# Kernel optimization log

Measured on AMD Instinct MI355X. Metric: run time of the kernel, lower is better.

The kernel has to match this reference:

```python
import jax, jax.numpy as jnp
import numpy as np

N_NODES = 50000
N_EDGES = 800000
D_IN = 128
D_HID = 128
N_CLS = 40


def setup_inputs() -> dict:
    key = jax.random.key(0)
    ks = jax.random.split(key, 9)
    x = jax.random.normal(ks[0], (N_NODES, D_IN), dtype=jnp.float32)
    edge_index = jax.random.randint(ks[1], (2, N_EDGES), 0, N_NODES, dtype=jnp.int64)
    def lin(k, fan_in, fan_out):
        bound = 1.0 / np.sqrt(fan_in)
        return jax.random.uniform(k, (fan_in, fan_out), jnp.float32, -bound, bound)
    params = {
        'w1_l': lin(ks[2], D_IN, D_HID), 'w1_r': lin(ks[3], D_IN, D_HID),
        'b1': jnp.zeros((D_HID,), jnp.float32),
        'w2_l': lin(ks[4], D_HID, D_HID), 'w2_r': lin(ks[5], D_HID, D_HID),
        'b2': jnp.zeros((D_HID,), jnp.float32),
        'w3_l': lin(ks[6], D_HID, N_CLS), 'w3_r': lin(ks[7], D_HID, N_CLS),
        'b3': jnp.zeros((N_CLS,), jnp.float32),
    }
    return {'x': x, 'edge_index': edge_index, **params}


def _sage_layer(x, src, dst, w_l, w_r, b):
    # mean-aggregate messages from src -> dst, then lin_l(agg) + lin_r(x) + b, relu
    msgs = x[src]                                             # [E, d] gather
    agg = jax.ops.segment_sum(msgs, dst, num_segments=x.shape[0])  # [N, d]
    deg = jax.ops.segment_sum(jnp.ones((src.shape[0],), x.dtype), dst,
                              num_segments=x.shape[0])        # [N]
    agg = agg / jnp.maximum(deg, 1.0)[:, None]
    out = agg @ w_l + x @ w_r + b
    return jax.nn.relu(out)  # dropout p=0.0 -> identity


def reference(x, edge_index, w1_l, w1_r, b1, w2_l, w2_r, b2, w3_l, w3_r, b3):
    src, dst = edge_index[0], edge_index[1]
    h = _sage_layer(x, src, dst, w1_l, w1_r, b1)
    h = _sage_layer(h, src, dst, w2_l, w2_r, b2)
    h = _sage_layer(h, src, dst, w3_l, w3_r, b3)
    return h
```

## Files before the change

kernel.cpp:

```cpp
#include <hip/hip_runtime.h>
#include <hip/hip_bf16.h>

#define NN 50000
#define NE 800000
#define DD 128
#define NCLS 40
#define NBK ((NN + 255) >> 8)
#define EPB 1024
#define PB ((NE + EPB - 1) / EPB)
#define CVB ((NN * DD / 4) / 256)
#define WB 384
#define SEMAX 5120

typedef _Float16 f16x8 __attribute__((ext_vector_type(8)));
typedef _Float16 f16x4 __attribute__((ext_vector_type(4)));
typedef float f32x4 __attribute__((ext_vector_type(4)));

__device__ __forceinline__ unsigned int pack2h(_Float16 a, _Float16 b) {
    union { _Float16 h[2]; unsigned int u; } c;
    c.h[0] = a; c.h[1] = b;
    return c.u;
}
__device__ __forceinline__ void unpack2h(unsigned int p, float& a, float& b) {
    union { unsigned int u; _Float16 h[2]; } c;
    c.u = p;
    a = (float)c.h[0]; b = (float)c.h[1];
}

__global__ void k_front(const int* __restrict__ ei, int* __restrict__ cellcnt,
                        int* __restrict__ celloff, unsigned int* __restrict__ pairs,
                        const float* __restrict__ x, unsigned short* __restrict__ xh,
                        const float* __restrict__ w1l, const float* __restrict__ w1r,
                        const float* __restrict__ w2l, const float* __restrict__ w2r,
                        const float* __restrict__ w3l, const float* __restrict__ w3r,
                        unsigned short* __restrict__ bt1h,
                        unsigned short* __restrict__ bt2h,
                        unsigned short* __restrict__ bt3h) {
    if (blockIdx.x >= PB + CVB) {
        int idx = blockIdx.x - (PB + CVB);
        int w = idx >> 1, half = idx & 1;
        int ks = w & 7, tmp = w >> 3;
        int nt = tmp & 7, layer = tmp >> 3;
        const int NT = (layer == 2) ? 3 : 8;
        const int NC = (layer == 2) ? NCLS : DD;
        if (nt >= NT) return;
        const float* wl = (layer == 0) ? w1l : (layer == 1) ? w2l : w3l;
        const float* wr = (layer == 0) ? w1r : (layer == 1) ? w2r : w3r;
        unsigned short* bh = (layer == 0) ? bt1h : (layer == 1) ? bt2h : bt3h;
        int t = threadIdx.x;
        int j = t & 7, lane = (t >> 3) + half * 32;
        int row = nt * 16 + (lane & 15);
        int k = ks * 32 + (lane >> 4) * 8 + j;
        float v = 0.f;
        if (row < NC)
            v = (k < 128) ? wl[(size_t)k * NC + row] : wr[(size_t)(k - 128) * NC + row];
        union { _Float16 f; unsigned short u; } ch;
        ch.f = (_Float16)v;
        bh[((size_t)(ks * NT + nt) * 64 + lane) * 8 + j] = ch.u;
        return;
    }
    if (blockIdx.x >= PB) {
        int i = (blockIdx.x - PB) * 256 + threadIdx.x;
        float4 v = ((const float4*)x)[i];
        f16x4 h;
        h[0] = (_Float16)v.x; h[1] = (_Float16)v.y;
        h[2] = (_Float16)v.z; h[3] = (_Float16)v.w;
        *(f16x4*)(xh + (size_t)i * 4) = h;
        return;
    }
    __shared__ int hist[NBK];
    __shared__ int s[256];
    __shared__ unsigned int sE[EPB];
    __shared__ int nz;
    const int t = threadIdx.x, blk = blockIdx.x;
    const int e0 = blk * EPB;
    if (t == 0) nz = 0;
    for (int i = t; i < NBK; i += 256) hist[i] = 0;
    __syncthreads();
    int any = 0;
    for (int i = t; i < EPB; i += 256)
        if (ei[2 * e0 + 2 * i + 1] != 0) any = 1;
    if (any) atomicOr(&nz, 1);
    __syncthreads();
    const int is64 = (nz == 0);
    unsigned int v[EPB / 256];
    int eb[EPB / 256], er[EPB / 256];
#pragma unroll
    for (int j = 0; j < EPB / 256; ++j) {
        int e = e0 + j * 256 + t;
        if (e < NE) {
            int sv, d;
            if (is64) { sv = ei[2 * e]; d = ei[2 * (NE + e)]; }
            else      { sv = ei[e];     d = ei[NE + e]; }
            v[j] = ((unsigned)sv << 16) | (unsigned)d;
            eb[j] = d >> 8;
            er[j] = atomicAdd(&hist[eb[j]], 1);
        } else {
            eb[j] = -1;
        }
    }
    __syncthreads();
    int hv = (t < NBK) ? hist[t] : 0;
    s[t] = hv;
    __syncthreads();
#pragma unroll
    for (int off = 1; off < 256; off <<= 1) {
        int u = (t >= off) ? s[t - off] : 0;
        __syncthreads();
        s[t] += u;
        __syncthreads();
    }
#pragma unroll
    for (int j = 0; j < EPB / 256; ++j)
        if (eb[j] >= 0) sE[s[eb[j]] - hist[eb[j]] + er[j]] = v[j];
    __syncthreads();
    ((uint4*)(pairs + (size_t)blk * EPB))[t] = ((const uint4*)sE)[t];
    for (int i = t; i < NBK; i += 256) {
        cellcnt[(size_t)i * PB + blk] = hist[i];
        celloff[(size_t)i * PB + blk] = s[i] - hist[i];
    }
}

__global__ void k_scan_ba(const int* __restrict__ cellcnt, int* __restrict__ bsum) {
    __shared__ int red[256];
    int b = blockIdx.x, t = threadIdx.x;
    int acc = 0;
    for (int i = t; i < PB; i += 256) acc += cellcnt[(size_t)b * PB + i];
    red[t] = acc;
    __syncthreads();
#pragma unroll
    for (int off = 128; off > 0; off >>= 1) {
        if (t < off) red[t] += red[t + off];
        __syncthreads();
    }
    if (t == 0) bsum[b] = red[0];
}

__global__ void k_fill2(const unsigned int* __restrict__ pairs,
                        const int* __restrict__ cellcnt,
                        const int* __restrict__ celloff,
                        const int* __restrict__ bsum,
                        int* __restrict__ row_ptr, int* __restrict__ srcs) {
    __shared__ unsigned int sE[SEMAX];
    __shared__ int hist[256];
    __shared__ int cur[256];
    __shared__ int sb[256];
    __shared__ int scnt;
    const int b = blockIdx.x, t = threadIdx.x;
    if (t < 256) {
        int v = (t < NBK) ? bsum[t] : 0;
        sb[t] = v;
    }
    if (t == 0) scnt = 0;
    if (t < 256) hist[t] = 0;
    __syncthreads();
#pragma unroll
    for (int off = 1; off < 256; off <<= 1) {
        int u = (t >= off && t < 256) ? sb[t - off] : 0;
        __syncthreads();
        if (t < 256) sb[t] += u;
        __syncthreads();
    }
    const int bbase = (b == 0) ? 0 : sb[b - 1];
    if (b == NBK - 1 && t == 0) row_ptr[NN] = sb[NBK - 1];
    for (int blk = t; blk < PB; blk += 512) {
        int cnt = cellcnt[(size_t)b * PB + blk];
        if (cnt) {
            int off = celloff[(size_t)b * PB + blk];
            int base = atomicAdd(&scnt, cnt);
            if (base + cnt <= SEMAX) {
                const unsigned int* pp = pairs + (size_t)blk * EPB + off;
                for (int j = 0; j < cnt; ++j) {
                    unsigned int v = pp[j];
                    sE[base + j] = v;
                    atomicAdd(&hist[v & 255u], 1);
                }
            }
        }
    }
    __syncthreads();
    int h = (t < 256) ? hist[t] : 0;
    if (t < 256) cur[t] = h;
    __syncthreads();
#pragma unroll
    for (int off = 1; off < 256; off <<= 1) {
        int u = (t >= off && t < 256) ? cur[t - off] : 0;
        __syncthreads();
        if (t < 256) cur[t] += u;
        __syncthreads();
    }
    if (t < 256) {
        int node = (b << 8) + t;
        int base = bbase + cur[t] - h;
        if (node < NN) row_ptr[node] = base;
        cur[t] = base;
    }
    __syncthreads();
    int total = min(scnt, SEMAX);
    for (int i = t; i < total; i += 512) {
        unsigned int v = sE[i];
        int pos = atomicAdd(&cur[v & 255u], 1);
        srcs[pos] = (int)(v >> 16);
    }
}

__global__ void k_agg(const unsigned int* __restrict__ inh, const int* __restrict__ row_ptr,
                      const int* __restrict__ srcs, unsigned int* __restrict__ oh) {
    int node = blockIdx.x * 4 + (threadIdx.x >> 6);
    if (node >= NN) return;
    int lane = threadIdx.x & 63;
    int b = row_ptr[node], e = row_ptr[node + 1];
    float a0 = 0.f, a1 = 0.f;
    int nfull = (e - b) & ~7;
    int i = b;
    for (; i < b + nfull; i += 8) {
        unsigned int p0 = inh[(size_t)srcs[i + 0] * 64 + lane];
        unsigned int p1 = inh[(size_t)srcs[i + 1] * 64 + lane];
        unsigned int p2 = inh[(size_t)srcs[i + 2] * 64 + lane];
        unsigned int p3 = inh[(size_t)srcs[i + 3] * 64 + lane];
        unsigned int p4 = inh[(size_t)srcs[i + 4] * 64 + lane];
        unsigned int p5 = inh[(size_t)srcs[i + 5] * 64 + lane];
        unsigned int p6 = inh[(size_t)srcs[i + 6] * 64 + lane];
        unsigned int p7 = inh[(size_t)srcs[i + 7] * 64 + lane];
        float u0, u1;
        unpack2h(p0, u0, u1); a0 += u0; a1 += u1;
        unpack2h(p1, u0, u1); a0 += u0; a1 += u1;
        unpack2h(p2, u0, u1); a0 += u0; a1 += u1;
        unpack2h(p3, u0, u1); a0 += u0; a1 += u1;
        unpack2h(p4, u0, u1); a0 += u0; a1 += u1;
        unpack2h(p5, u0, u1); a0 += u0; a1 += u1;
        unpack2h(p6, u0, u1); a0 += u0; a1 += u1;
        unpack2h(p7, u0, u1); a0 += u0; a1 += u1;
    }
    int rem = e - i;
    if (rem > 0) {
        unsigned int p[8];
#pragma unroll
        for (int j = 0; j < 8; ++j) {
            int idx = i + j;
            if (idx > e - 1) idx = e - 1;
            p[j] = inh[(size_t)srcs[idx] * 64 + lane];
        }
#pragma unroll
        for (int j = 0; j < 8; ++j) {
            float u0, u1;
            unpack2h(p[j], u0, u1);
            if (j < rem) { a0 += u0; a1 += u1; }
        }
    }
    int deg = e - b;
    float inv = 1.0f / (float)(deg > 0 ? deg : 1);
    oh[(size_t)node * 64 + lane] = pack2h((_Float16)(a0 * inv), (_Float16)(a1 * inv));
}

template <int NT, int KPS, bool PACKOUT>
__launch_bounds__(256, 4)
__global__ void k_mfma(const unsigned short* __restrict__ A1h,
                       const unsigned short* __restrict__ A2h,
                       const unsigned short* __restrict__ Bthf,
                       const float* __restrict__ bias, float* __restrict__ outf,
                       unsigned short* __restrict__ outh, const int NC) {
    constexpr int STAGE_ELEMS = KPS * NT * 64 * 8;
    constexpr int STAGE_U4 = STAGE_ELEMS / 8;
    __shared__ unsigned short sBh[STAGE_ELEMS];

    const int tid = threadIdx.x;
    const int wave = tid >> 6, lane = tid & 63;
    const int quad = lane >> 4, mr = lane & 15;
    const int m0 = blockIdx.x * 64 + wave * 16;
    const int row = m0 + mr;
    const bool rok = row < NN;

    f32x4 acc[NT] = {};
    const f16x8 zero = {};

    auto aload = [&](int ks) -> f16x8 {
        const int ko = ((ks * 32) & 127) + quad * 8;
        const unsigned short* base = (ks < 4) ? A1h : A2h;
        return rok ? *(const f16x8*)(base + (size_t)row * 128 + ko) : zero;
    };

    f16x8 cah = aload(0), pah;

#pragma unroll
    for (int s = 0; s < 8 / KPS; ++s) {
        const uint4* gh = (const uint4*)(Bthf + (size_t)s * STAGE_ELEMS);
        uint4* lh = (uint4*)sBh;
        if (s) __syncthreads();
        for (int i = tid; i < STAGE_U4; i += 256) lh[i] = gh[i];
        __syncthreads();

#pragma unroll
        for (int kl = 0; kl < KPS; ++kl) {
            const int ks = s * KPS + kl;
            if (ks < 7) pah = aload(ks + 1);
#pragma unroll
            for (int n = 0; n < NT; ++n) {
                const int fo = ((kl * NT + n) * 64 + lane) * 8;
                f16x8 bh = *(const f16x8*)(sBh + fo);
                acc[n] = __builtin_amdgcn_mfma_f32_16x16x32_f16(cah, bh, acc[n], 0, 0, 0);
            }
            cah = pah;
        }
    }

#pragma unroll
    for (int n = 0; n < NT; ++n) {
        int col = n * 16 + mr;
        float bv = (col < NC) ? bias[col] : 0.f;
#pragma unroll
        for (int r = 0; r < 4; ++r) {
            int orow = m0 + quad * 4 + r;
            if (orow < NN && col < NC) {
                float v = acc[n][r] + bv;
                v = v > 0.f ? v : 0.f;
                if (PACKOUT) {
                    union { _Float16 f; unsigned short u; } ch;
                    ch.f = (_Float16)v;
                    outh[(size_t)orow * 128 + col] = ch.u;
                } else {
                    outf[(size_t)orow * NC + col] = v;
                }
            }
        }
    }
}

extern "C" void kernel_launch(void* const* d_in, const int* in_sizes, int n_in,
                              void* d_out, int out_size, void* d_ws, size_t ws_size,
                              hipStream_t stream) {
    const float* x    = (const float*)d_in[0];
    const int*   ei   = (const int*)d_in[1];
    const float* w1_l = (const float*)d_in[2];
    const float* w1_r = (const float*)d_in[3];
    const float* b1   = (const float*)d_in[4];
    const float* w2_l = (const float*)d_in[5];
    const float* w2_r = (const float*)d_in[6];
    const float* b2   = (const float*)d_in[7];
    const float* w3_l = (const float*)d_in[8];
    const float* w3_r = (const float*)d_in[9];
    const float* b3   = (const float*)d_in[10];
    float* out = (float*)d_out;

    char* w = (char*)d_ws;
    size_t off = 0;
    auto alloc = [&](size_t bytes) -> void* {
        void* p = w + off;
        off += (bytes + 255) / 256 * 256;
        return p;
    };
    int* row_ptr = (int*)alloc((size_t)(NN + 1) * 4);
    int* srcs    = (int*)alloc((size_t)NE * 4);
    int* cellcnt = (int*)alloc((size_t)NBK * PB * 4);
    int* celloff = (int*)alloc((size_t)NBK * PB * 4);
    int* bsum    = (int*)alloc((size_t)NBK * 4);
    unsigned int* pairs = (unsigned int*)alloc((size_t)PB * EPB * 4);
    unsigned short* xh   = (unsigned short*)alloc((size_t)NN * DD * 2);
    unsigned short* aggh = (unsigned short*)alloc((size_t)NN * DD * 2);
    unsigned short* h1h  = (unsigned short*)alloc((size_t)NN * DD * 2);
    unsigned short* bt1h = (unsigned short*)alloc((size_t)8 * 8 * 64 * 8 * 2);
    unsigned short* bt2h = (unsigned short*)alloc((size_t)8 * 8 * 64 * 8 * 2);
    unsigned short* bt3h = (unsigned short*)alloc((size_t)8 * 3 * 64 * 8 * 2);
    unsigned short* h2h = xh;
    (void)ws_size;

    k_front<<<PB + CVB + WB, 256, 0, stream>>>(ei, cellcnt, celloff, pairs, x, xh,
                                               w1_l, w1_r, w2_l, w2_r, w3_l, w3_r,
                                               bt1h, bt2h, bt3h);
    k_scan_ba<<<NBK, 256, 0, stream>>>(cellcnt, bsum);
    k_fill2<<<NBK, 512, 0, stream>>>(pairs, cellcnt, celloff, bsum, row_ptr, srcs);

    const int gmb = (NN + 63) / 64;
    const int gab = (NN + 3) / 4;
    k_agg<<<gab, 256, 0, stream>>>((const unsigned int*)xh, row_ptr, srcs,
                                   (unsigned int*)aggh);
    k_mfma<8, 4, true><<<gmb, 256, 0, stream>>>(aggh, xh, bt1h, b1,
                                                nullptr, h1h, DD);
    k_agg<<<gab, 256, 0, stream>>>((const unsigned int*)h1h, row_ptr, srcs,
                                   (unsigned int*)aggh);
    k_mfma<8, 4, true><<<gmb, 256, 0, stream>>>(aggh, h1h, bt2h, b2,
                                                nullptr, h2h, DD);
    k_agg<<<gab, 256, 0, stream>>>((const unsigned int*)h2h, row_ptr, srcs,
                                   (unsigned int*)aggh);
    k_mfma<3, 4, false><<<gmb, 256, 0, stream>>>(aggh, h2h, bt3h, b3,
                                                 out, nullptr, NCLS);
}
```

Measured before the change: 243.6 us.

## Fuse aggregation with GEMM for layers 1-2 and reorder layer 3 transform-then-aggregate

Layers 1 and 2 now aggregate neighbour features into shared memory and immediately run the MFMA GEMM in the same kernel, which removes the write and re-read of the aggregated buffer and one launch per layer. Layer 3 uses linearity: it first projects h2 down to 40 classes (padded to 64 in fp16) for both weight matrices, then gathers the narrow projected rows and adds the self term, bias and relu. The 128-wide gather shrinks to 64 fp16 values per edge. The fused kernel does serial per-wave aggregation of 16 nodes before the GEMM, which may lower latency hiding and parallelism, and layer 3 now rounds the projection to fp16 before averaging.

```diff
diff --git a/kernel.cpp b/kernel.cpp
--- a/kernel.cpp
+++ b/kernel.cpp
@@ -204,66 +204,130 @@
     }
 }
 
-__global__ void k_agg(const unsigned int* __restrict__ inh, const int* __restrict__ row_ptr,
-                      const int* __restrict__ srcs, unsigned int* __restrict__ oh) {
-    int node = blockIdx.x * 4 + (threadIdx.x >> 6);
-    if (node >= NN) return;
-    int lane = threadIdx.x & 63;
-    int b = row_ptr[node], e = row_ptr[node + 1];
-    float a0 = 0.f, a1 = 0.f;
-    int nfull = (e - b) & ~7;
-    int i = b;
-    for (; i < b + nfull; i += 8) {
-        unsigned int p0 = inh[(size_t)srcs[i + 0] * 64 + lane];
-        unsigned int p1 = inh[(size_t)srcs[i + 1] * 64 + lane];
-        unsigned int p2 = inh[(size_t)srcs[i + 2] * 64 + lane];
-        unsigned int p3 = inh[(size_t)srcs[i + 3] * 64 + lane];
-        unsigned int p4 = inh[(size_t)srcs[i + 4] * 64 + lane];
-        unsigned int p5 = inh[(size_t)srcs[i + 5] * 64 + lane];
-        unsigned int p6 = inh[(size_t)srcs[i + 6] * 64 + lane];
-        unsigned int p7 = inh[(size_t)srcs[i + 7] * 64 + lane];
-        float u0, u1;
-        unpack2h(p0, u0, u1); a0 += u0; a1 += u1;
-        unpack2h(p1, u0, u1); a0 += u0; a1 += u1;
-        unpack2h(p2, u0, u1); a0 += u0; a1 += u1;
-        unpack2h(p3, u0, u1); a0 += u0; a1 += u1;
-        unpack2h(p4, u0, u1); a0 += u0; a1 += u1;
-        unpack2h(p5, u0, u1); a0 += u0; a1 += u1;
-        unpack2h(p6, u0, u1); a0 += u0; a1 += u1;
-        unpack2h(p7, u0, u1); a0 += u0; a1 += u1;
-    }
-    int rem = e - i;
-    if (rem > 0) {
-        unsigned int p[8];
-#pragma unroll
-        for (int j = 0; j < 8; ++j) {
-            int idx = i + j;
-            if (idx > e - 1) idx = e - 1;
-            p[j] = inh[(size_t)srcs[idx] * 64 + lane];
-        }
-#pragma unroll
-        for (int j = 0; j < 8; ++j) {
-            float u0, u1;
-            unpack2h(p[j], u0, u1);
-            if (j < rem) { a0 += u0; a1 += u1; }
-        }
-    }
-    int deg = e - b;
-    float inv = 1.0f / (float)(deg > 0 ? deg : 1);
-    oh[(size_t)node * 64 + lane] = pack2h((_Float16)(a0 * inv), (_Float16)(a1 * inv));
-}
-
-template <int NT, int KPS, bool PACKOUT>
-__launch_bounds__(256, 4)
-__global__ void k_mfma(const unsigned short* __restrict__ A1h,
-                       const unsigned short* __restrict__ A2h,
-                       const unsigned short* __restrict__ Bthf,
-                       const float* __restrict__ bias, float* __restrict__ outf,
-                       unsigned short* __restrict__ outh, const int NC) {
-    constexpr int STAGE_ELEMS = KPS * NT * 64 * 8;
-    constexpr int STAGE_U4 = STAGE_ELEMS / 8;
-    __shared__ unsigned short sBh[STAGE_ELEMS];
-
+__global__ __launch_bounds__(256, 4)
+void k_fuse(const unsigned int* __restrict__ inh, const int* __restrict__ row_ptr,
+            const int* __restrict__ srcs, const unsigned short* __restrict__ Bthf,
+            const float* __restrict__ bias, unsigned short* __restrict__ outh) {
+    __shared__ unsigned int sAu[64 * 68];
+    __shared__ unsigned short sBh[2 * 8 * 64 * 8];
+
+    const int tid = threadIdx.x;
+    const int wave = tid >> 6, lane = tid & 63;
+    const int quad = lane >> 4, mr = lane & 15;
+    const int m0b = blockIdx.x * 64;
+    const int nw0 = m0b + wave * 16;
+
+    int rp = row_ptr[min(nw0 + min(lane, 16), NN)];
+    for (int ni = 0; ni < 16; ++ni) {
+        int node = nw0 + ni;
+        unsigned int packed = 0u;
+        if (node < NN) {
+            int b = __shfl(rp, ni), e = __shfl(rp, ni + 1);
+            float a0 = 0.f, a1 = 0.f;
+            int nfull = (e - b) & ~7;
+            int i = b;
+            for (; i < b + nfull; i += 8) {
+                unsigned int p0 = inh[(size_t)srcs[i + 0] * 64 + lane];
+                unsigned int p1 = inh[(size_t)srcs[i + 1] * 64 + lane];
+                unsigned int p2 = inh[(size_t)srcs[i + 2] * 64 + lane];
+                unsigned int p3 = inh[(size_t)srcs[i + 3] * 64 + lane];
+                unsigned int p4 = inh[(size_t)srcs[i + 4] * 64 + lane];
+                unsigned int p5 = inh[(size_t)srcs[i + 5] * 64 + lane];
+                unsigned int p6 = inh[(size_t)srcs[i + 6] * 64 + lane];
+                unsigned int p7 = inh[(size_t)srcs[i + 7] * 64 + lane];
+                float u0, u1;
+                unpack2h(p0, u0, u1); a0 += u0; a1 += u1;
+                unpack2h(p1, u0, u1); a0 += u0; a1 += u1;
+                unpack2h(p2, u0, u1); a0 += u0; a1 += u1;
+                unpack2h(p3, u0, u1); a0 += u0; a1 += u1;
+                unpack2h(p4, u0, u1); a0 += u0; a1 += u1;
+                unpack2h(p5, u0, u1); a0 += u0; a1 += u1;
+                unpack2h(p6, u0, u1); a0 += u0; a1 += u1;
+                unpack2h(p7, u0, u1); a0 += u0; a1 += u1;
+            }
+            int rem = e - i;
+            if (rem > 0) {
+                unsigned int p[8];
+#pragma unroll
+                for (int j = 0; j < 8; ++j) {
+                    int idx = i + j;
+                    if (idx > e - 1) idx = e - 1;
+                    p[j] = inh[(size_t)srcs[idx] * 64 + lane];
+                }
+#pragma unroll
+                for (int j = 0; j < 8; ++j) {
+                    float u0, u1;
+                    unpack2h(p[j], u0, u1);
+                    if (j < rem) { a0 += u0; a1 += u1; }
+                }
+            }
+            int deg = e - b;
+            float inv = 1.0f / (float)(deg > 0 ? deg : 1);
+            packed = pack2h((_Float16)(a0 * inv), (_Float16)(a1 * inv));
+        }
+        sAu[(wave * 16 + ni) * 68 + lane] = packed;
+    }
+
+    const unsigned short* inh16 = (const unsigned short*)inh;
+    const int row = nw0 + mr;
+    const bool rok = row < NN;
+    const f16x8 zero = {};
+    f16x8 self[4];
+#pragma unroll
+    for (int j = 0; j < 4; ++j)
+        self[j] = rok ? *(const f16x8*)(inh16 + (size_t)row * 128 + j * 32 + quad * 8)
+                      : zero;
+
+    f32x4 acc[8] = {};
+    const int arow = (wave * 16 + mr) * 68;
+
+#pragma unroll
+    for (int s = 0; s < 4; ++s) {
+        const uint4* gh = (const uint4*)(Bthf + (size_t)s * (2 * 8 * 64 * 8));
+        uint4* lh = (uint4*)sBh;
+        if (s) __syncthreads();
+        for (int i = tid; i < 1024; i += 256) lh[i] = gh[i];
+        __syncthreads();
+#pragma unroll
+        for (int kl = 0; kl < 2; ++kl) {
+            const int ks = s * 2 + kl;
+            f16x8 ah;
+            if (ks < 4)
+                ah = *(const f16x8*)(&sAu[arow + ks * 16 + quad * 4]);
+            else
+                ah = self[ks - 4];
+#pragma unroll
+            for (int n = 0; n < 8; ++n) {
+                f16x8 bh = *(const f16x8*)(sBh + ((kl * 8 + n) * 64 + lane) * 8);
+                acc[n] = __builtin_amdgcn_mfma_f32_16x16x32_f16(ah, bh, acc[n], 0, 0, 0);
+            }
+        }
+    }
+
+#pragma unroll
+    for (int n = 0; n < 8; ++n) {
+        int col = n * 16 + mr;
+        float bv = bias[col];
+#pragma unroll
+        for (int r = 0; r < 4; ++r) {
+            int orow = nw0 + quad * 4 + r;
+            if (orow < NN) {
+                float v = acc[n][r] + bv;
+                v = v > 0.f ? v : 0.f;
+                union { _Float16 f; unsigned short u; } ch;
+                ch.f = (_Float16)v;
+                outh[(size_t)orow * 128 + col] = ch.u;
+            }
+        }
+    }
+}
+
+__global__ __launch_bounds__(256, 4)
+void k_gemm3(const unsigned short* __restrict__ Ah,
+             const unsigned short* __restrict__ Bthf,
+             const float* __restrict__ bias,
+             unsigned short* __restrict__ zh, float* __restrict__ yf) {
+    __shared__ unsigned short sBh[8 * 3 * 64 * 8];
     const int tid = threadIdx.x;
     const int wave = tid >> 6, lane = tid & 63;
     const int quad = lane >> 4, mr = lane & 15;
@@ -271,58 +335,83 @@
     const int row = m0 + mr;
     const bool rok = row < NN;
 
-    f32x4 acc[NT] = {};
+    const uint4* gh = (const uint4*)Bthf;
+    uint4* lh = (uint4*)sBh;
+    for (int i = tid; i < (8 * 3 * 64 * 8) / 8; i += 256) lh[i] = gh[i];
+
     const f16x8 zero = {};
-
-    auto aload = [&](int ks) -> f16x8 {
-        const int ko = ((ks * 32) & 127) + quad * 8;
-        const unsigned short* base = (ks < 4) ? A1h : A2h;
-        return rok ? *(const f16x8*)(base + (size_t)row * 128 + ko) : zero;
-    };
-
-    f16x8 cah = aload(0), pah;
-
-#pragma unroll
-    for (int s = 0; s < 8 / KPS; ++s) {
-        const uint4* gh = (const uint4*)(Bthf + (size_t)s * STAGE_ELEMS);
-        uint4* lh = (uint4*)sBh;
-        if (s) __syncthreads();
-        for (int i = tid; i < STAGE_U4; i += 256) lh[i] = gh[i];
-        __syncthreads();
-
-#pragma unroll
-        for (int kl = 0; kl < KPS; ++kl) {
-            const int ks = s * KPS + kl;
-            if (ks < 7) pah = aload(ks + 1);
-#pragma unroll
-            for (int n = 0; n < NT; ++n) {
-                const int fo = ((kl * NT + n) * 64 + lane) * 8;
-                f16x8 bh = *(const f16x8*)(sBh + fo);
-                acc[n] = __builtin_amdgcn_mfma_f32_16x16x32_f16(cah, bh, acc[n], 0, 0, 0);
-            }
-            cah = pah;
-        }
-    }
-
-#pragma unroll
-    for (int n = 0; n < NT; ++n) {
+    f16x8 a[4];
+#pragma unroll
+    for (int j = 0; j < 4; ++j)
+        a[j] = rok ? *(const f16x8*)(Ah + (size_t)row * 128 + j * 32 + quad * 8)
+                   : zero;
+    __syncthreads();
+
+    f32x4 accl[3] = {}, accr[3] = {};
+#pragma unroll
+    for (int ks = 0; ks < 4; ++ks) {
+#pragma unroll
+        for (int n = 0; n < 3; ++n) {
+            f16x8 bl = *(const f16x8*)(sBh + ((ks * 3 + n) * 64 + lane) * 8);
+            accl[n] = __builtin_amdgcn_mfma_f32_16x16x32_f16(a[ks], bl, accl[n], 0, 0, 0);
+            f16x8 br = *(const f16x8*)(sBh + (((ks + 4) * 3 + n) * 64 + lane) * 8);
+            accr[n] = __builtin_amdgcn_mfma_f32_16x16x32_f16(a[ks], br, accr[n], 0, 0, 0);
+        }
+    }
+
+#pragma unroll
+    for (int n = 0; n < 3; ++n) {
         int col = n * 16 + mr;
-        float bv = (col < NC) ? bias[col] : 0.f;
+        float bv = (col < NCLS) ? bias[col] : 0.f;
 #pragma unroll
         for (int r = 0; r < 4; ++r) {
             int orow = m0 + quad * 4 + r;
-            if (orow < NN && col < NC) {
-                float v = acc[n][r] + bv;
-                v = v > 0.f ? v : 0.f;
-                if (PACKOUT) {
-                    union { _Float16 f; unsigned short u; } ch;
-                    ch.f = (_Float16)v;
-                    outh[(size_t)orow * 128 + col] = ch.u;
-                } else {
-                    outf[(size_t)orow * NC + col] = v;
-                }
-            }
-        }
+            if (orow < NN) {
+                union { _Float16 f; unsigned short u; } ch;
+                ch.f = (_Float16)accl[n][r];
+                zh[(size_t)orow * 64 + col] = ch.u;
+                if (col < NCLS) yf[(size_t)orow * 40 + col] = accr[n][r] + bv;
+            }
+        }
+    }
+}
+
+__global__ void k_agg3(const unsigned int* __restrict__ zu,
+                       const int* __restrict__ row_ptr,
+                       const int* __restrict__ srcs,
+                       const float* __restrict__ yf, float* __restrict__ out) {
+    const int tid = threadIdx.x;
+    const int wave = tid >> 6, lane = tid & 63;
+    const int half = lane >> 5, hl = lane & 31;
+    const int node = blockIdx.x * 8 + wave * 2 + half;
+    int b = row_ptr[node], e = row_ptr[node + 1];
+    int deg = e - b;
+    int od = __shfl_xor(deg, 32);
+    int md = max(deg, od);
+    int ce = (e > b) ? (e - 1) : b;
+    float a0 = 0.f, a1 = 0.f;
+    for (int base = 0; base < md; base += 8) {
+        unsigned int p[8];
+#pragma unroll
+        for (int j = 0; j < 8; ++j) {
+            int idx = b + base + j;
+            if (idx > ce) idx = ce;
+            p[j] = zu[(size_t)srcs[idx] * 32 + hl];
+        }
+#pragma unroll
+        for (int j = 0; j < 8; ++j) {
+            float u0, u1;
+            unpack2h(p[j], u0, u1);
+            if (base + j < deg) { a0 += u0; a1 += u1; }
+        }
+    }
+    float inv = 1.0f / (float)(deg > 0 ? deg : 1);
+    if (hl < 20) {
+        float2 yv = ((const float2*)yf)[(size_t)node * 20 + hl];
+        float2 o;
+        o.x = fmaxf(a0 * inv + yv.x, 0.f);
+        o.y = fmaxf(a1 * inv + yv.y, 0.f);
+        ((float2*)out)[(size_t)node * 20 + hl] = o;
     }
 }
 
@@ -356,8 +445,9 @@
     int* bsum    = (int*)alloc((size_t)NBK * 4);
     unsigned int* pairs = (unsigned int*)alloc((size_t)PB * EPB * 4);
     unsigned short* xh   = (unsigned short*)alloc((size_t)NN * DD * 2);
-    unsigned short* aggh = (unsigned short*)alloc((size_t)NN * DD * 2);
     unsigned short* h1h  = (unsigned short*)alloc((size_t)NN * DD * 2);
+    unsigned short* zh   = (unsigned short*)alloc((size_t)NN * 64 * 2);
+    float*          yf   = (float*)alloc((size_t)NN * 40 * 4);
     unsigned short* bt1h = (unsigned short*)alloc((size_t)8 * 8 * 64 * 8 * 2);
     unsigned short* bt2h = (unsigned short*)alloc((size_t)8 * 8 * 64 * 8 * 2);
     unsigned short* bt3h = (unsigned short*)alloc((size_t)8 * 3 * 64 * 8 * 2);
@@ -371,17 +461,11 @@
     k_fill2<<<NBK, 512, 0, stream>>>(pairs, cellcnt, celloff, bsum, row_ptr, srcs);
 
     const int gmb = (NN + 63) / 64;
-    const int gab = (NN + 3) / 4;
-    k_agg<<<gab, 256, 0, stream>>>((const unsigned int*)xh, row_ptr, srcs,
-                                   (unsigned int*)aggh);
-    k_mfma<8, 4, true><<<gmb, 256, 0, stream>>>(aggh, xh, bt1h, b1,
-                                                nullptr, h1h, DD);
-    k_agg<<<gab, 256, 0, stream>>>((const unsigned int*)h1h, row_ptr, srcs,
-                                   (unsigned int*)aggh);
-    k_mfma<8, 4, true><<<gmb, 256, 0, stream>>>(aggh, h1h, bt2h, b2,
-                                                nullptr, h2h, DD);
-    k_agg<<<gab, 256, 0, stream>>>((const unsigned int*)h2h, row_ptr, srcs,
-                                   (unsigned int*)aggh);
-    k_mfma<3, 4, false><<<gmb, 256, 0, stream>>>(aggh, h2h, bt3h, b3,
-                                                 out, nullptr, NCLS);
-}
+    k_fuse<<<gmb, 256, 0, stream>>>((const unsigned int*)xh, row_ptr, srcs,
+                                    bt1h, b1, h1h);
+    k_fuse<<<gmb, 256, 0, stream>>>((const unsigned int*)h1h, row_ptr, srcs,
+                                    bt2h, b2, h2h);
+    k_gemm3<<<gmb, 256, 0, stream>>>(h2h, bt3h, b3, zh, yf);
+    k_agg3<<<NN / 8, 256, 0, stream>>>((const unsigned int*)zh, row_ptr, srcs,
+                                       yf, out);
+}
```

Result: slower. 251.0 us (+3.0%).

## Project layer-3 features before aggregation and widen gather unroll to 16

Applied to the files above, without the earlier changes.

Layer 3 now multiplies h2 by W3_l and W3_r first, writing a 64-wide fp16 projection (40 classes padded) and an fp32 self term with bias. It then averages the projected rows over neighbours, adds the self term and applies relu. This uses linearity of the mean to shrink the gathered row from 128 to 64 halves, cutting the memory traffic of the last gather. The generic aggregation kernel also unrolls 16 loads per iteration instead of 8 and gets an occupancy hint. The cost is an extra intermediate write and read, and fp16 rounding of the projected values before averaging.

```diff
diff --git a/kernel.cpp b/kernel.cpp
--- a/kernel.cpp
+++ b/kernel.cpp
@@ -204,45 +204,39 @@
     }
 }
 
-__global__ void k_agg(const unsigned int* __restrict__ inh, const int* __restrict__ row_ptr,
-                      const int* __restrict__ srcs, unsigned int* __restrict__ oh) {
+__global__ __launch_bounds__(256, 8)
+void k_agg(const unsigned int* __restrict__ inh, const int* __restrict__ row_ptr,
+           const int* __restrict__ srcs, unsigned int* __restrict__ oh) {
     int node = blockIdx.x * 4 + (threadIdx.x >> 6);
     if (node >= NN) return;
     int lane = threadIdx.x & 63;
     int b = row_ptr[node], e = row_ptr[node + 1];
     float a0 = 0.f, a1 = 0.f;
-    int nfull = (e - b) & ~7;
     int i = b;
-    for (; i < b + nfull; i += 8) {
-        unsigned int p0 = inh[(size_t)srcs[i + 0] * 64 + lane];
-        unsigned int p1 = inh[(size_t)srcs[i + 1] * 64 + lane];
-        unsigned int p2 = inh[(size_t)srcs[i + 2] * 64 + lane];
-        unsigned int p3 = inh[(size_t)srcs[i + 3] * 64 + lane];
-        unsigned int p4 = inh[(size_t)srcs[i + 4] * 64 + lane];
-        unsigned int p5 = inh[(size_t)srcs[i + 5] * 64 + lane];
-        unsigned int p6 = inh[(size_t)srcs[i + 6] * 64 + lane];
-        unsigned int p7 = inh[(size_t)srcs[i + 7] * 64 + lane];
-        float u0, u1;
-        unpack2h(p0, u0, u1); a0 += u0; a1 += u1;
-        unpack2h(p1, u0, u1); a0 += u0; a1 += u1;
-        unpack2h(p2, u0, u1); a0 += u0; a1 += u1;
-        unpack2h(p3, u0, u1); a0 += u0; a1 += u1;
-        unpack2h(p4, u0, u1); a0 += u0; a1 += u1;
-        unpack2h(p5, u0, u1); a0 += u0; a1 += u1;
-        unpack2h(p6, u0, u1); a0 += u0; a1 += u1;
-        unpack2h(p7, u0, u1); a0 += u0; a1 += u1;
+    for (; i + 16 <= e; i += 16) {
+        unsigned int p[16];
+#pragma unroll
+        for (int j = 0; j < 16; ++j)
+            p[j] = inh[(size_t)srcs[i + j] * 64 + lane];
+#pragma unroll
+        for (int j = 0; j < 16; ++j) {
+            float u0, u1;
+            unpack2h(p[j], u0, u1);
+            a0 += u0; a1 += u1;
+        }
     }
     int rem = e - i;
     if (rem > 0) {
-        unsigned int p[8];
-#pragma unroll
-        for (int j = 0; j < 8; ++j) {
+        int ce = e - 1;
+        unsigned int p[16];
+#pragma unroll
+        for (int j = 0; j < 16; ++j) {
             int idx = i + j;
-            if (idx > e - 1) idx = e - 1;
+            if (idx > ce) idx = ce;
             p[j] = inh[(size_t)srcs[idx] * 64 + lane];
         }
 #pragma unroll
-        for (int j = 0; j < 8; ++j) {
+        for (int j = 0; j < 16; ++j) {
             float u0, u1;
             unpack2h(p[j], u0, u1);
             if (j < rem) { a0 += u0; a1 += u1; }
@@ -323,6 +317,100 @@
                 }
             }
         }
+    }
+}
+
+__global__ __launch_bounds__(256, 4)
+void k_gemm3(const unsigned short* __restrict__ Ah,
+             const unsigned short* __restrict__ Bthf,
+             const float* __restrict__ bias,
+             unsigned short* __restrict__ zh, float* __restrict__ yf) {
+    __shared__ unsigned short sBh[8 * 3 * 64 * 8];
+    const int tid = threadIdx.x;
+    const int wave = tid >> 6, lane = tid & 63;
+    const int quad = lane >> 4, mr = lane & 15;
+    const int m0 = blockIdx.x * 64 + wave * 16;
+    const int row = m0 + mr;
+    const bool rok = row < NN;
+
+    const uint4* gh = (const uint4*)Bthf;
+    uint4* lh = (uint4*)sBh;
+    for (int i = tid; i < (8 * 3 * 64 * 8) / 8; i += 256) lh[i] = gh[i];
+
+    const f16x8 zero = {};
+    f16x8 a[4];
+#pragma unroll
+    for (int j = 0; j < 4; ++j)
+        a[j] = rok ? *(const f16x8*)(Ah + (size_t)row * 128 + j * 32 + quad * 8)
+                   : zero;
+    __syncthreads();
+
+    f32x4 accl[3] = {}, accr[3] = {};
+#pragma unroll
+    for (int ks = 0; ks < 4; ++ks) {
+#pragma unroll
+        for (int n = 0; n < 3; ++n) {
+            f16x8 bl = *(const f16x8*)(sBh + ((ks * 3 + n) * 64 + lane) * 8);
+            accl[n] = __builtin_amdgcn_mfma_f32_16x16x32_f16(a[ks], bl, accl[n], 0, 0, 0);
+            f16x8 br = *(const f16x8*)(sBh + (((ks + 4) * 3 + n) * 64 + lane) * 8);
+            accr[n] = __builtin_amdgcn_mfma_f32_16x16x32_f16(a[ks], br, accr[n], 0, 0, 0);
+        }
+    }
+
+#pragma unroll
+    for (int n = 0; n < 3; ++n) {
+        int col = n * 16 + mr;
+        float bv = (col < NCLS) ? bias[col] : 0.f;
+#pragma unroll
+        for (int r = 0; r < 4; ++r) {
+            int orow = m0 + quad * 4 + r;
+            if (orow < NN) {
+                union { _Float16 f; unsigned short u; } ch;
+                ch.f = (_Float16)accl[n][r];
+                zh[(size_t)orow * 64 + col] = ch.u;
+                if (col < NCLS) yf[(size_t)orow * 40 + col] = accr[n][r] + bv;
+            }
+        }
+    }
+}
+
+__global__ __launch_bounds__(256, 8)
+void k_agg3(const unsigned int* __restrict__ zu,
+            const int* __restrict__ row_ptr,
+            const int* __restrict__ srcs,
+            const float* __restrict__ yf, float* __restrict__ out) {
+    const int tid = threadIdx.x;
+    const int wave = tid >> 6, lane = tid & 63;
+    const int half = lane >> 5, hl = lane & 31;
+    const int node = blockIdx.x * 8 + wave * 2 + half;
+    int b = row_ptr[node], e = row_ptr[node + 1];
+    int deg = e - b;
+    int od = __shfl_xor(deg, 32);
+    int md = max(deg, od);
+    int ce = (e > b) ? (e - 1) : b;
+    float a0 = 0.f, a1 = 0.f;
+    for (int base = 0; base < md; base += 16) {
+        unsigned int p[16];
+#pragma unroll
+        for (int j = 0; j < 16; ++j) {
+            int idx = b + base + j;
+            if (idx > ce) idx = ce;
+            p[j] = zu[(size_t)srcs[idx] * 32 + hl];
+        }
+#pragma unroll
+        for (int j = 0; j < 16; ++j) {
+            float u0, u1;
+            unpack2h(p[j], u0, u1);
+            if (base + j < deg) { a0 += u0; a1 += u1; }
+        }
+    }
+    float inv = 1.0f / (float)(deg > 0 ? deg : 1);
+    if (hl < 20) {
+        float2 yv = ((const float2*)yf)[(size_t)node * 20 + hl];
+        float2 o;
+        o.x = fmaxf(a0 * inv + yv.x, 0.f);
+        o.y = fmaxf(a1 * inv + yv.y, 0.f);
+        ((float2*)out)[(size_t)node * 20 + hl] = o;
     }
 }
 
@@ -358,6 +446,8 @@
     unsigned short* xh   = (unsigned short*)alloc((size_t)NN * DD * 2);
     unsigned short* aggh = (unsigned short*)alloc((size_t)NN * DD * 2);
     unsigned short* h1h  = (unsigned short*)alloc((size_t)NN * DD * 2);
+    unsigned short* zh   = (unsigned short*)alloc((size_t)NN * 64 * 2);
+    float*          yf   = (float*)alloc((size_t)NN * 40 * 4);
     unsigned short* bt1h = (unsigned short*)alloc((size_t)8 * 8 * 64 * 8 * 2);
     unsigned short* bt2h = (unsigned short*)alloc((size_t)8 * 8 * 64 * 8 * 2);
     unsigned short* bt3h = (unsigned short*)alloc((size_t)8 * 3 * 64 * 8 * 2);
@@ -380,8 +470,7 @@
                                    (unsigned int*)aggh);
     k_mfma<8, 4, true><<<gmb, 256, 0, stream>>>(aggh, h1h, bt2h, b2,
                                                 nullptr, h2h, DD);
-    k_agg<<<gab, 256, 0, stream>>>((const unsigned int*)h2h, row_ptr, srcs,
-                                   (unsigned int*)aggh);
-    k_mfma<3, 4, false><<<gmb, 256, 0, stream>>>(aggh, h2h, bt3h, b3,
-                                                 out, nullptr, NCLS);
-}
+    k_gemm3<<<gmb, 256, 0, stream>>>(h2h, bt3h, b3, zh, yf);
+    k_agg3<<<NN / 8, 256, 0, stream>>>((const unsigned int*)zh, row_ptr, srcs,
+                                       yf, out);
+}
```

Measured after the change: 232.7 us. 4.5% less time.
